# Optimization experiments

Hardware: AMD Instinct MI355X
Metric: run time of the kernel (lower is better)

The kernel has to match this reference:

```python
import jax, jax.numpy as jnp
import numpy as np

B, S, H = 256, 1024, 256
DIMS = [1, 16, 16, 12, 8, 4, 4, 1]  # CNN MLP layer widths


def setup_inputs() -> dict:
    key = jax.random.key(0)
    ks = jax.random.split(key, 32)
    inp = {"x": jax.random.normal(ks[0], (B, S, 1), jnp.float32)}
    for idx, (din, dout) in enumerate(zip(DIMS[:-1], DIMS[1:])):
        inp[f"w{idx+1}"] = jax.random.normal(ks[1 + idx], (dout, din), jnp.float32) / np.sqrt(din).astype(np.float32)
        inp[f"b{idx+1}"] = jnp.zeros((dout,), jnp.float32)
    gdim = 1 + H  # input_dim + hidden_dim
    for j, name in enumerate(["f", "i", "g", "o"]):
        inp[f"w_{name}"] = jax.random.normal(ks[10 + j], (H, gdim), jnp.float32) / np.sqrt(gdim).astype(np.float32)
        inp[f"b_{name}"] = jnp.zeros((H,), jnp.float32)
    inp["w_head"] = jax.random.normal(ks[20], (1, H), jnp.float32) / np.sqrt(H).astype(np.float32)
    inp["b_head"] = jnp.zeros((1,), jnp.float32)
    return inp


def reference(x, w1, b1, w2, b2, w3, b3, w4, b4, w5, b5, w6, b6, w7, b7,
              w_f, b_f, w_i, b_i, w_g, b_g, w_o, b_o, w_head, b_head):
    batch, seq_len, _ = x.shape
    # CNN-style MLP applied per timestep (flattened over batch*seq)
    h = x.reshape(batch * seq_len, 1)
    for w, b in [(w1, b1), (w2, b2), (w3, b3), (w4, b4), (w5, b5), (w6, b6)]:
        h = jnp.tanh(h @ w.T + b)
    cnn_features = (h @ w7.T + b7).reshape(batch, seq_len, 1)

    # ClassicalQLSTM over time-major sequence (S, B, 1)
    seq = cnn_features.transpose(1, 0, 2)

    def step(carry, xt):
        hx, cx = carry
        comb = jnp.concatenate([xt, hx], axis=1)  # (B, 1+H)
        f = jax.nn.sigmoid(comb @ w_f.T + b_f)
        i = jax.nn.sigmoid(comb @ w_i.T + b_i)
        g = jnp.tanh(comb @ w_g.T + b_g)
        o = jax.nn.sigmoid(comb @ w_o.T + b_o)
        cx = f * cx + i * g
        hx = o * jnp.tanh(cx)
        return (hx, cx), None

    init = (jnp.zeros((batch, w_f.shape[0]), x.dtype), jnp.zeros((batch, w_f.shape[0]), x.dtype))
    (hx, _), _ = jax.lax.scan(step, init, seq)
    logits = hx @ w_head.T + b_head
    return cnn_features, logits
```

## Files before the change

kernel.cpp:

```cpp
#include <hip/hip_runtime.h>

#define BATCH 256
#define SEQ   1024
#define HID   256
#define NU    4
#define UNITS 64
#define BB    4
#define NBG   64
#define NKG   8
#define KPG   32

typedef float f32x4 __attribute__((ext_vector_type(4)));

__device__ __forceinline__ float tanh_fast(float x) {
    float e = __expf(2.0f * x);
    return 1.0f - 2.0f / (e + 1.0f);
}
__device__ __forceinline__ float sigmoid_fast(float x) {
    return 1.0f / (1.0f + __expf(-x));
}

template<int DIN, int DOUT, bool ACT>
__device__ __forceinline__ void dense(const float* __restrict__ w,
                                      const float* __restrict__ b,
                                      const float* hin, float* hout) {
    #pragma unroll
    for (int i = 0; i < DOUT; i++) {
        float a = b[i];
        #pragma unroll
        for (int j = 0; j < DIN; j++) a = fmaf(w[i * DIN + j], hin[j], a);
        hout[i] = ACT ? tanh_fast(a) : a;
    }
}

__global__ __launch_bounds__(256) void mlp_kernel(
    const float* __restrict__ x,
    const float* __restrict__ w1, const float* __restrict__ b1,
    const float* __restrict__ w2, const float* __restrict__ b2,
    const float* __restrict__ w3, const float* __restrict__ b3,
    const float* __restrict__ w4, const float* __restrict__ b4,
    const float* __restrict__ w5, const float* __restrict__ b5,
    const float* __restrict__ w6, const float* __restrict__ b6,
    const float* __restrict__ w7, const float* __restrict__ b7,
    float* __restrict__ cnn_out)
{
    int n = blockIdx.x * 256 + threadIdx.x;
    float h0[1] = { x[n] };
    float h1[16], h2[16], h3[12], h4[8], h5[4], h6[4], h7[1];
    dense<1, 16, true >(w1, b1, h0, h1);
    dense<16, 16, true >(w2, b2, h1, h2);
    dense<16, 12, true >(w3, b3, h2, h3);
    dense<12, 8, true >(w4, b4, h3, h4);
    dense<8, 4, true >(w5, b5, h4, h5);
    dense<4, 4, true >(w6, b6, h5, h6);
    dense<4, 1, false>(w7, b7, h6, h7);
    cnn_out[n] = h7[0];
}

__global__ __launch_bounds__(256) void pack_kernel(
    const float* __restrict__ wf, const float* __restrict__ wi,
    const float* __restrict__ wg, const float* __restrict__ wo,
    f32x4* __restrict__ wpack)
{
    int j = threadIdx.x;
    int k = blockIdx.x;
    int src = j * 257 + k;
    f32x4 v = { wf[src], wi[src], wg[src], wo[src] };
    wpack[k * 256 + j] = v;
}

#define GATE_FMA(W, HV)                      \
    acc[0] = fmaf((W)[0], (HV), acc[0]);     \
    acc[1] = fmaf((W)[1], (HV), acc[1]);     \
    acc[2] = fmaf((W)[2], (HV), acc[2]);     \
    acc[3] = fmaf((W)[3], (HV), acc[3]);

#define LOADX4(dst, ptr)                                              \
    asm volatile("global_load_dwordx4 %0, %1, off"                    \
                 : "=v"(dst) : "v"(ptr) : "memory")

#define PIN4(v) asm volatile("" : "+v"(v))

__global__
__attribute__((amdgpu_waves_per_eu(2, 2)))
__launch_bounds__(512) void lstm_kernel(
    const float* __restrict__ xB,
    const f32x4* __restrict__ wpack,
    const float* __restrict__ bf, const float* __restrict__ bi,
    const float* __restrict__ bg_, const float* __restrict__ bo,
    const float* __restrict__ w_head, const float* __restrict__ b_head,
    float* __restrict__ logits,
    unsigned long long* __restrict__ hglob)
{
    __shared__ f32x4 partial[NKG][BB][UNITS];
    __shared__ __align__(16) float hx_s[BB][HID];
    __shared__ float xlds[BB * SEQ];

    const int bid = blockIdx.x;
    const int u   = bid >> 6;
    const int bgp = bid & 63;
    const int tid = threadIdx.x;
    const int kg  = tid >> 6;
    const int j   = tid & 63;
    const int unit = u * UNITS + j;

    f32x4 wreg[KPG];
    #pragma unroll
    for (int i = 0; i < KPG; i++) {
        const f32x4* p = wpack + (1 + kg * KPG + i) * HID + unit;
        LOADX4(wreg[i], p);
    }
    f32x4 w0;
    {
        const f32x4* p = wpack + unit;
        LOADX4(w0, p);
    }
    asm volatile("s_waitcnt vmcnt(0)" ::: "memory");
    f32x4 bias = { bf[unit], bi[unit], bg_[unit], bo[unit] };
    PIN4(bias);

    #pragma unroll
    for (int i = 0; i < 8; i++)
        xlds[i * 512 + tid] = xB[(bgp * BB) * SEQ + i * 512 + tid];
    ((float*)hx_s)[tid] = 0.0f;
    ((float*)hx_s)[tid + 512] = 0.0f;

    float cx = 0.0f, hj = 0.0f;
    const int b2 = tid >> 6;
    __syncthreads();

    for (int t = 0; t < SEQ; ++t) {
        #pragma unroll
        for (int bb = 0; bb < BB; ++bb) {
            f32x4 acc = { 0.f, 0.f, 0.f, 0.f };
            const f32x4* h4 = (const f32x4*)&hx_s[bb][kg * KPG];
            #pragma unroll
            for (int q = 0; q < KPG / 4; ++q) {
                f32x4 h = h4[q];
                GATE_FMA(wreg[4 * q + 0], h[0]);
                GATE_FMA(wreg[4 * q + 1], h[1]);
                GATE_FMA(wreg[4 * q + 2], h[2]);
                GATE_FMA(wreg[4 * q + 3], h[3]);
            }
            partial[kg][bb][j] = acc;
        }
        __syncthreads();

        float hnew = 0.0f;
        if (tid < 256) {
            f32x4 acc = partial[0][b2][j];
            #pragma unroll
            for (int g = 1; g < NKG; ++g) {
                f32x4 p = partial[g][b2][j];
                acc[0] += p[0]; acc[1] += p[1]; acc[2] += p[2]; acc[3] += p[3];
            }
            float xt = xlds[b2 * 1024 + t];
            float pf = fmaf(w0[0], xt, acc[0] + bias[0]);
            float pi = fmaf(w0[1], xt, acc[1] + bias[1]);
            float pg = fmaf(w0[2], xt, acc[2] + bias[2]);
            float po = fmaf(w0[3], xt, acc[3] + bias[3]);
            float f  = sigmoid_fast(pf);
            float i  = sigmoid_fast(pi);
            float g  = tanh_fast(pg);
            float o  = sigmoid_fast(po);
            cx = fmaf(f, cx, i * g);
            hnew = o * tanh_fast(cx);
            hj = hnew;
        }

        if (t < SEQ - 1) {
            const int par = t & 1;
            if (tid < 256) {
                unsigned long long pk =
                    ((unsigned long long)(unsigned)(t + 1) << 32) |
                    (unsigned long long)__float_as_uint(hnew);
                __hip_atomic_store(&hglob[(size_t)par * (256 * 256) + bid * 256 + tid],
                                   pk, __ATOMIC_RELAXED, __HIP_MEMORY_SCOPE_SYSTEM);
                hx_s[b2][u * UNITS + j] = hnew;
            }
            asm volatile("" ::: "memory");
            for (int r = tid; r < 768; r += 512) {
                const int s  = r >> 8;
                const int su = (u + 1 + s) & 3;
                const int rr = r & 255;
                const unsigned long long* p =
                    hglob + (size_t)par * (256 * 256) + (su * NBG + bgp) * 256 + rr;
                unsigned long long v;
                do {
                    v = __hip_atomic_load(p, __ATOMIC_RELAXED,
                                          __HIP_MEMORY_SCOPE_SYSTEM);
                } while ((int)(v >> 32) != t + 1);
                hx_s[rr >> 6][su * UNITS + (rr & 63)] =
                    __uint_as_float((unsigned)(v & 0xffffffffull));
            }
            __syncthreads();
        } else {
            if (tid < 256) hx_s[b2][u * UNITS + j] = hnew;
        }
    }

    __syncthreads();
    float* red = (float*)partial;
    if (tid < 256) red[tid] = w_head[unit] * hj;
    __syncthreads();
    #pragma unroll
    for (int off = 32; off > 0; off >>= 1) {
        if (tid < 256 && (tid & 63) < off) red[tid] += red[tid + off];
        __syncthreads();
    }
    if (tid < 256 && (tid & 63) == 0) {
        float sum = red[tid] + (u == 0 ? b_head[0] : 0.0f);
        atomicAdd(&logits[bgp * BB + (tid >> 6)], sum);
    }
}

extern "C" void kernel_launch(void* const* d_in, const int* in_sizes, int n_in,
                              void* d_out, int out_size, void* d_ws, size_t ws_size,
                              hipStream_t stream) {
    const float* x      = (const float*)d_in[0];
    const float* w1     = (const float*)d_in[1];
    const float* b1     = (const float*)d_in[2];
    const float* w2     = (const float*)d_in[3];
    const float* b2     = (const float*)d_in[4];
    const float* w3     = (const float*)d_in[5];
    const float* b3     = (const float*)d_in[6];
    const float* w4     = (const float*)d_in[7];
    const float* b4     = (const float*)d_in[8];
    const float* w5     = (const float*)d_in[9];
    const float* b5     = (const float*)d_in[10];
    const float* w6     = (const float*)d_in[11];
    const float* b6     = (const float*)d_in[12];
    const float* w7     = (const float*)d_in[13];
    const float* b7     = (const float*)d_in[14];
    const float* w_f    = (const float*)d_in[15];
    const float* b_f    = (const float*)d_in[16];
    const float* w_i    = (const float*)d_in[17];
    const float* b_i    = (const float*)d_in[18];
    const float* w_g    = (const float*)d_in[19];
    const float* b_g    = (const float*)d_in[20];
    const float* w_o    = (const float*)d_in[21];
    const float* b_o    = (const float*)d_in[22];
    const float* w_head = (const float*)d_in[23];
    const float* b_head = (const float*)d_in[24];

    float* out    = (float*)d_out;
    float* logits = out + BATCH * SEQ;

    char* ws = (char*)d_ws;
    f32x4* wpack = (f32x4*)ws;
    unsigned long long* hglob =
        (unsigned long long*)(ws + 1052672);

    hipMemsetAsync(hglob, 0, 2 * 256 * 256 * sizeof(unsigned long long), stream);
    hipMemsetAsync(logits, 0, 256 * sizeof(float), stream);
    pack_kernel<<<257, 256, 0, stream>>>(w_f, w_i, w_g, w_o, wpack);
    mlp_kernel<<<(BATCH * SEQ) / 256, 256, 0, stream>>>(
        x, w1, b1, w2, b2, w3, b3, w4, b4, w5, b5, w6, b6, w7, b7, out);

    void* args[] = { (void*)&out, (void*)&wpack,
                     (void*)&b_f, (void*)&b_i, (void*)&b_g, (void*)&b_o,
                     (void*)&w_head, (void*)&b_head,
                     (void*)&logits, (void*)&hglob };
    hipLaunchCooperativeKernel((void*)lstm_kernel, dim3(256), dim3(512),
                               args, 0, stream);
}
```

Baseline: 3.111 ms.

## Split recurrent weights between LDS and per-step global streaming, fuse batch loop

Recurrent weights no longer stay resident in registers. The first 14 rows per k-group are held in LDS, and the remaining 18 rows are reloaded from global memory (cache) on every timestep. The batch loop is interchanged so each weight row is reused across all four batch rows with four accumulators, and the x input is read from global per step instead of being staged in LDS. This frees registers and the x LDS buffer, but it adds per-step global and LDS weight traffic on the serial critical path.

```diff
diff --git a/kernel.cpp b/kernel.cpp
--- a/kernel.cpp
+++ b/kernel.cpp
@@ -9,6 +9,8 @@
 #define NBG   64
 #define NKG   8
 #define KPG   32
+#define LROWS 14
+#define SROWS 18
 
 typedef float f32x4 __attribute__((ext_vector_type(4)));
 
@@ -69,17 +71,11 @@
     wpack[k * 256 + j] = v;
 }
 
-#define GATE_FMA(W, HV)                      \
-    acc[0] = fmaf((W)[0], (HV), acc[0]);     \
-    acc[1] = fmaf((W)[1], (HV), acc[1]);     \
-    acc[2] = fmaf((W)[2], (HV), acc[2]);     \
-    acc[3] = fmaf((W)[3], (HV), acc[3]);
-
-#define LOADX4(dst, ptr)                                              \
-    asm volatile("global_load_dwordx4 %0, %1, off"                    \
-                 : "=v"(dst) : "v"(ptr) : "memory")
-
-#define PIN4(v) asm volatile("" : "+v"(v))
+#define GFMA(A, W, HV)                       \
+    (A)[0] = fmaf((W)[0], (HV), (A)[0]);     \
+    (A)[1] = fmaf((W)[1], (HV), (A)[1]);     \
+    (A)[2] = fmaf((W)[2], (HV), (A)[2]);     \
+    (A)[3] = fmaf((W)[3], (HV), (A)[3]);
 
 __global__
 __attribute__((amdgpu_waves_per_eu(2, 2)))
@@ -92,9 +88,9 @@
     float* __restrict__ logits,
     unsigned long long* __restrict__ hglob)
 {
+    __shared__ f32x4 wlds[NKG][LROWS][UNITS];
     __shared__ f32x4 partial[NKG][BB][UNITS];
     __shared__ __align__(16) float hx_s[BB][HID];
-    __shared__ float xlds[BB * SEQ];
 
     const int bid = blockIdx.x;
     const int u   = bid >> 6;
@@ -104,61 +100,68 @@
     const int j   = tid & 63;
     const int unit = u * UNITS + j;
 
-    f32x4 wreg[KPG];
     #pragma unroll
-    for (int i = 0; i < KPG; i++) {
-        const f32x4* p = wpack + (1 + kg * KPG + i) * HID + unit;
-        LOADX4(wreg[i], p);
-    }
-    f32x4 w0;
-    {
-        const f32x4* p = wpack + unit;
-        LOADX4(w0, p);
-    }
-    asm volatile("s_waitcnt vmcnt(0)" ::: "memory");
-    f32x4 bias = { bf[unit], bi[unit], bg_[unit], bo[unit] };
-    PIN4(bias);
-
-    #pragma unroll
-    for (int i = 0; i < 8; i++)
-        xlds[i * 512 + tid] = xB[(bgp * BB) * SEQ + i * 512 + tid];
+    for (int i = 0; i < LROWS; ++i)
+        wlds[kg][i][j] = wpack[(1 + kg * KPG + i) * HID + unit];
+
+    const f32x4* wstream = wpack + (size_t)(1 + kg * KPG + LROWS) * HID + unit;
+    const f32x4 w0   = wpack[unit];
+    const f32x4 bias = { bf[unit], bi[unit], bg_[unit], bo[unit] };
+
     ((float*)hx_s)[tid] = 0.0f;
     ((float*)hx_s)[tid + 512] = 0.0f;
 
     float cx = 0.0f, hj = 0.0f;
     const int b2 = tid >> 6;
+    const int xrow = (bgp * BB + (tid >> 6)) * SEQ;
     __syncthreads();
 
     for (int t = 0; t < SEQ; ++t) {
-        #pragma unroll
-        for (int bb = 0; bb < BB; ++bb) {
-            f32x4 acc = { 0.f, 0.f, 0.f, 0.f };
-            const f32x4* h4 = (const f32x4*)&hx_s[bb][kg * KPG];
+        float xt = 0.0f;
+        if (tid < 256) xt = xB[xrow + t];
+
+        f32x4 wst[SROWS];
+        #pragma unroll
+        for (int s = 0; s < SROWS; ++s) wst[s] = wstream[(size_t)s * HID];
+
+        f32x4 acc[BB];
+        #pragma unroll
+        for (int bb = 0; bb < BB; ++bb) acc[bb] = (f32x4){0.f, 0.f, 0.f, 0.f};
+
+        const f32x4* h0p = (const f32x4*)&hx_s[0][kg * KPG];
+        const f32x4* h1p = (const f32x4*)&hx_s[1][kg * KPG];
+        const f32x4* h2p = (const f32x4*)&hx_s[2][kg * KPG];
+        const f32x4* h3p = (const f32x4*)&hx_s[3][kg * KPG];
+
+        #pragma unroll
+        for (int q = 0; q < KPG / 4; ++q) {
+            f32x4 ha = h0p[q], hb = h1p[q], hc = h2p[q], hd = h3p[q];
             #pragma unroll
-            for (int q = 0; q < KPG / 4; ++q) {
-                f32x4 h = h4[q];
-                GATE_FMA(wreg[4 * q + 0], h[0]);
-                GATE_FMA(wreg[4 * q + 1], h[1]);
-                GATE_FMA(wreg[4 * q + 2], h[2]);
-                GATE_FMA(wreg[4 * q + 3], h[3]);
-            }
-            partial[kg][bb][j] = acc;
+            for (int e = 0; e < 4; ++e) {
+                const int k = q * 4 + e;
+                f32x4 w = (k < LROWS) ? wlds[kg][k][j] : wst[k - LROWS];
+                GFMA(acc[0], w, ha[e]);
+                GFMA(acc[1], w, hb[e]);
+                GFMA(acc[2], w, hc[e]);
+                GFMA(acc[3], w, hd[e]);
+            }
         }
+        #pragma unroll
+        for (int bb = 0; bb < BB; ++bb) partial[kg][bb][j] = acc[bb];
         __syncthreads();
 
         float hnew = 0.0f;
         if (tid < 256) {
-            f32x4 acc = partial[0][b2][j];
+            f32x4 a = partial[0][b2][j];
             #pragma unroll
             for (int g = 1; g < NKG; ++g) {
                 f32x4 p = partial[g][b2][j];
-                acc[0] += p[0]; acc[1] += p[1]; acc[2] += p[2]; acc[3] += p[3];
-            }
-            float xt = xlds[b2 * 1024 + t];
-            float pf = fmaf(w0[0], xt, acc[0] + bias[0]);
-            float pi = fmaf(w0[1], xt, acc[1] + bias[1]);
-            float pg = fmaf(w0[2], xt, acc[2] + bias[2]);
-            float po = fmaf(w0[3], xt, acc[3] + bias[3]);
+                a[0] += p[0]; a[1] += p[1]; a[2] += p[2]; a[3] += p[3];
+            }
+            float pf = fmaf(w0[0], xt, a[0] + bias[0]);
+            float pi = fmaf(w0[1], xt, a[1] + bias[1]);
+            float pg = fmaf(w0[2], xt, a[2] + bias[2]);
+            float po = fmaf(w0[3], xt, a[3] + bias[3]);
             float f  = sigmoid_fast(pf);
             float i  = sigmoid_fast(pi);
             float g  = tanh_fast(pg);
```

Result: slower. 5.124 ms (+64.7%).
